# Performance work log

Measured on AMD Instinct MI355X. Metric: run time of the kernel, lower is better.

## Reference

```python
import jax, jax.numpy as jnp
import numpy as np
from jax import lax


def conv2d(x, w, b, pad):
    out = lax.conv_general_dilated(x, w, (1, 1), [(pad, pad), (pad, pad)],
                                   dimension_numbers=('NCHW', 'OIHW', 'NCHW'))
    return out + b[None, :, None, None]


def deform_conv3x3(src, offset, weight, bias):
    # torchvision.ops.deform_conv2d, 3x3 kernel, stride 1, pad 1, no mask.
    # src [B,C,H,W]; offset [B,18,H,W] laid out (y,x) per kernel pos, row-major.
    B, C, H, W = src.shape
    off = offset.reshape(B, 9, 2, H, W)
    ky, kx = jnp.meshgrid(jnp.arange(3) - 1, jnp.arange(3) - 1, indexing='ij')
    ky = ky.reshape(9).astype(src.dtype)
    kx = kx.reshape(9).astype(src.dtype)
    yy = jnp.arange(H, dtype=src.dtype)[:, None]
    xx = jnp.arange(W, dtype=src.dtype)[None, :]
    py = yy[None, None] + ky[None, :, None, None] + off[:, :, 0]  # [B,9,H,W]
    px = xx[None, None] + kx[None, :, None, None] + off[:, :, 1]
    y0 = jnp.floor(py)
    x0 = jnp.floor(px)
    wy1 = py - y0
    wx1 = px - x0

    def gather(yi, xi):
        valid = ((yi >= 0) & (yi < H) & (xi >= 0) & (xi < W)).astype(src.dtype)
        yc = jnp.clip(yi, 0, H - 1).astype(jnp.int32)
        xc = jnp.clip(xi, 0, W - 1).astype(jnp.int32)
        vals = jax.vmap(lambda s, a, c: s[:, a, c])(src, yc, xc)  # [B,C,9,H,W]
        return vals * valid[:, None]

    sampled = (gather(y0, x0) * ((1 - wy1) * (1 - wx1))[:, None]
               + gather(y0, x0 + 1) * ((1 - wy1) * wx1)[:, None]
               + gather(y0 + 1, x0) * (wy1 * (1 - wx1))[:, None]
               + gather(y0 + 1, x0 + 1) * (wy1 * wx1)[:, None])
    wk = weight.reshape(weight.shape[0], weight.shape[1], 9)
    return jnp.einsum('bckhw,ock->bohw', sampled, wk) + bias[None, :, None, None]


def setup_inputs() -> dict:
    key = jax.random.key(0)
    ks = jax.random.split(key, 16)
    B, C, H, W, N = 1, 256, 96, 96, 8
    current_feat = jax.random.normal(ks[0], (B, C, H, W), dtype=jnp.float32)
    neighbor_feats = jax.random.normal(ks[1], (N, B, C, H, W), dtype=jnp.float32)
    coord_diffs = jax.random.normal(ks[2], (N, 4), dtype=jnp.float32)
    align_w = jax.random.normal(ks[3], (C, C, 3, 3), dtype=jnp.float32) * 0.02
    align_b = jax.random.normal(ks[4], (C,), dtype=jnp.float32) * 0.02
    offset_w = jax.random.normal(ks[5], (18, 2 * C, 3, 3), dtype=jnp.float32) * 0.002
    offset_b = jax.random.normal(ks[6], (18,), dtype=jnp.float32) * 0.002
    gate1_w = jax.random.normal(ks[7], (C // 2, 2 * C, 3, 3), dtype=jnp.float32) * 0.02
    gate1_b = jax.random.normal(ks[8], (C // 2,), dtype=jnp.float32) * 0.02
    gate2_w = jax.random.normal(ks[9], (1, C // 2, 1, 1), dtype=jnp.float32) * 0.02
    gate2_b = jax.random.normal(ks[10], (1,), dtype=jnp.float32) * 0.02
    enc_w = jax.random.normal(ks[11], (C, 4), dtype=jnp.float32) * 0.1
    enc_b = jax.random.normal(ks[12], (C,), dtype=jnp.float32) * 0.1
    return dict(current_feat=current_feat, neighbor_feats=neighbor_feats,
                coord_diffs=coord_diffs, align_w=align_w, align_b=align_b,
                offset_w=offset_w, offset_b=offset_b, gate1_w=gate1_w,
                gate1_b=gate1_b, gate2_w=gate2_w, gate2_b=gate2_b,
                enc_w=enc_w, enc_b=enc_b)


def reference(current_feat, neighbor_feats, coord_diffs, align_w, align_b,
              offset_w, offset_b, gate1_w, gate1_b, gate2_w, gate2_b,
              enc_w, enc_b):
    B, C, H, W = current_feat.shape
    N = neighbor_feats.shape[0]
    aligned = []
    for n in range(N):  # fixed small neighbor set (<= 8)
        src = neighbor_feats[n]
        concat = jnp.concatenate([src, current_feat], axis=1)  # [B,2C,H,W]
        offset = conv2d(concat, offset_w, offset_b, 1)         # [B,18,H,W]
        aligned.append(deform_conv3x3(src, offset, align_w, align_b))
    all_feats = jnp.stack(aligned, axis=1)                     # [B,N,C,H,W]
    # coordinate embedding: Linear(4 -> C) per neighbor, shaped [1,N,C,1,1]
    coord_embs = (coord_diffs @ enc_w.T + enc_b)[None, :, :, None, None]
    cur_exp = jnp.broadcast_to(current_feat[:, None], (B, N, C, H, W))
    energy = jnp.concatenate([cur_exp, all_feats], axis=2).reshape(B * N, 2 * C, H, W)
    g = jax.nn.relu(conv2d(energy, gate1_w, gate1_b, 1))
    g = jax.nn.sigmoid(conv2d(g, gate2_w, gate2_b, 0))          # [B*N,1,H,W]
    weights = jax.nn.softmax(g.reshape(B, N, 1, H, W), axis=1)
    fused = (all_feats * weights + coord_embs).sum(axis=1)      # [B,C,H,W]
    return current_feat + 0.5 * fused
```

## Files before the change

kernel.cpp:

```cpp
#include <hip/hip_runtime.h>
#include <math.h>

#define CH   256
#define HH   96
#define WW   96
#define NN   8
#define HWSZ 9216
#define PLANE (HWSZ*CH)

typedef unsigned short u16;
typedef unsigned int   u32;
typedef short bf16x8 __attribute__((ext_vector_type(8)));
typedef float f32x4  __attribute__((ext_vector_type(4)));
typedef float f32x2  __attribute__((ext_vector_type(2)));

__device__ inline u16 f2bf(float f) {
    union { float f; u32 u; } v; v.f = f;
    u32 r = v.u + 0x7FFF + ((v.u >> 16) & 1);
    return (u16)(r >> 16);
}
__device__ inline float bflo(u32 u) {
    union { u32 u; float f; } v; v.u = u << 16; return v.f;
}
__device__ inline float bfhi(u32 u) {
    union { u32 u; float f; } v; v.u = u & 0xffff0000u; return v.f;
}
__device__ inline u32 pk2bf(float lo, float hi) {
    union { float f; u32 u; } a, b; a.f = lo; b.f = hi;
    u32 ra = a.u + 0x7FFF + ((a.u >> 16) & 1);
    u32 rb = b.u + 0x7FFF + ((b.u >> 16) & 1);
    return (ra >> 16) | (rb & 0xffff0000u);
}

__global__ void k_emb_sum(const float* __restrict__ cd,
                          const float* __restrict__ enc_w,
                          const float* __restrict__ enc_b,
                          float* __restrict__ emb)
{
    int c = threadIdx.x;
    float s = 0.f;
    for (int n = 0; n < NN; ++n) {
        float d = enc_b[c];
        #pragma unroll
        for (int j = 0; j < 4; ++j) d += cd[n*4 + j] * enc_w[c*4 + j];
        s += d;
    }
    emb[c] = s;
}

__global__ __launch_bounds__(256) void k_to_nhwc(const float* __restrict__ in,
                                                 u16* __restrict__ out)
{
    int n = blockIdx.y;
    int p0 = blockIdx.x * 64;
    int tid = threadIdx.x;
    __shared__ u16 T[64][262];

    int px4 = (tid & 15) * 4, cb = tid >> 4;
    for (int it = 0; it < 16; ++it) {
        int c = cb + it*16;
        float4 v = *reinterpret_cast<const float4*>(
            in + ((size_t)n*CH + c)*HWSZ + p0 + px4);
        T[px4+0][c] = f2bf(v.x);
        T[px4+1][c] = f2bf(v.y);
        T[px4+2][c] = f2bf(v.z);
        T[px4+3][c] = f2bf(v.w);
    }
    __syncthreads();
    int pxb = tid >> 5, ck = tid & 31;
    for (int it = 0; it < 8; ++it) {
        int p = pxb + it*8;
        *reinterpret_cast<int4*>(out + (size_t)n*PLANE + (size_t)(p0+p)*CH + ck*8) =
            *reinterpret_cast<const int4*>(&T[p][ck*8]);
    }
}

__global__ void k_pack_w(const float* __restrict__ w, u16* __restrict__ wp,
                         int O, int O_pad, int CIN, int order)
{
    int idx = blockIdx.x * 256 + threadIdx.x;
    int total = O_pad * CIN * 9;
    if (idx >= total) return;
    int o = idx / (CIN * 9);
    int K = idx % (CIN * 9);
    int tap = K / CIN, c = K % CIN;
    float v = (o < O) ? w[((size_t)o * CIN + c) * 9 + tap] : 0.f;
    int NKC = (CIN * 9) >> 5;
    int kc = order ? ((c >> 5)*9 + tap) : (tap*(CIN >> 5) + (c >> 5));
    int kl = c & 31;
    int lane = (kl >> 3) * 16 + (o & 15);
    size_t dstp = (((size_t)(o >> 4) * NKC + kc) * 64 + lane) * 8 + (kl & 7);
    wp[dstp] = f2bf(v);
}

template<int MTW, int EPI>
__global__ __launch_bounds__(512) void k_conv_nhwc(
    const u16* __restrict__ in0, long s0,
    const u16* __restrict__ in1, long s1,
    const u16* __restrict__ Wp, const float* __restrict__ b1,
    const float* __restrict__ g2w, const float* __restrict__ g2b,
    float* __restrict__ out)
{
    constexpr int NKC = 144, NCC = 16;
    int n = blockIdx.x, t = blockIdx.y;
    int tx0 = (t % 3) * 32, ty0 = (t / 3) * 8;
    int tid = threadIdx.x, lane = tid & 63, w = tid >> 6;
    int mh = w >> 2, pg = w & 3;
    int colq = lane >> 4;

    __shared__ __align__(16) u16 SB[340*40];
    __shared__ float gpart[8][64];

    f32x4 acc[MTW][4];
    #pragma unroll
    for (int mt = 0; mt < MTW; ++mt)
        #pragma unroll
        for (int nf = 0; nf < 4; ++nf)
            acc[mt][nf] = (f32x4){0.f,0.f,0.f,0.f};

    int bidx[4];
    #pragma unroll
    for (int nf = 0; nf < 4; ++nf) {
        int px = pg*64 + nf*16 + (lane & 15);
        int row = px >> 5, col = px & 31;
        bidx[nf] = ((row+1)*34 + (col+1))*40 + colq*8;
    }

    for (int cc = 0; cc < NCC; ++cc) {
        const u16* base = (cc < 8) ? in0 + (size_t)n*s0 + cc*32
                                   : in1 + (size_t)n*s1 + (cc-8)*32;
        for (int i = tid; i < 1360; i += 512) {
            int ph = i >> 2, q = i & 3;
            int r = ph / 34, col = ph - r*34;
            int y = ty0 - 1 + r, x = tx0 - 1 + col;
            bool v = ((unsigned)y < (unsigned)HH) && ((unsigned)x < (unsigned)WW);
            int off = v ? (y*WW + x)*CH : 0;
            int4 val = *reinterpret_cast<const int4*>(base + off + q*8);
            if (!v) val = make_int4(0,0,0,0);
            *reinterpret_cast<int4*>(&SB[ph*40 + q*8]) = val;
        }
        __syncthreads();
        #pragma unroll
        for (int tap = 0; tap < 9; ++tap) {
            int kc = tap*NCC + cc;
            bf16x8 a[MTW];
            #pragma unroll
            for (int mt = 0; mt < MTW; ++mt)
                a[mt] = *reinterpret_cast<const bf16x8*>(
                    Wp + (((size_t)(mh*MTW+mt)*NKC + kc)*64 + lane)*8);
            const int dy = tap/3 - 1, dx = tap%3 - 1;
            #pragma unroll
            for (int nf = 0; nf < 4; ++nf) {
                bf16x8 b = *reinterpret_cast<const bf16x8*>(
                    &SB[bidx[nf] + (dy*34 + dx)*40]);
                #pragma unroll
                for (int mt = 0; mt < MTW; ++mt)
                    acc[mt][nf] = __builtin_amdgcn_mfma_f32_16x16x32_bf16(
                                      a[mt], b, acc[mt][nf], 0, 0, 0);
            }
        }
        __syncthreads();
    }

    if (EPI == 0) {
        #pragma unroll
        for (int nf = 0; nf < 4; ++nf) {
            int px = pg*64 + nf*16 + (lane & 15);
            int gp = (ty0 + (px>>5))*WW + tx0 + (px & 31);
            #pragma unroll
            for (int mt = 0; mt < MTW; ++mt) {
                int o_base = (mh*MTW+mt)*16 + colq*4;
                #pragma unroll
                for (int r = 0; r < 4; ++r) {
                    int o = o_base + r;
                    if (o < 18)
                        out[((size_t)n*18 + o)*HWSZ + gp] = acc[mt][nf][r] + b1[o];
                }
            }
        }
    } else {
        float part[4];
        #pragma unroll
        for (int nf = 0; nf < 4; ++nf) {
            float s = 0.f;
            #pragma unroll
            for (int mt = 0; mt < MTW; ++mt) {
                int o_base = (mh*MTW+mt)*16 + colq*4;
                #pragma unroll
                for (int r = 0; r < 4; ++r) {
                    int o = o_base + r;
                    float vv = fmaxf(acc[mt][nf][r] + b1[o], 0.f);
                    s += vv * g2w[o];
                }
            }
            part[nf] = s;
        }
        #pragma unroll
        for (int nf = 0; nf < 4; ++nf) {
            part[nf] += __shfl_xor(part[nf], 16, 64);
            part[nf] += __shfl_xor(part[nf], 32, 64);
        }
        if (lane < 16) {
            #pragma unroll
            for (int nf = 0; nf < 4; ++nf)
                gpart[w][nf*16 + lane] = part[nf];
        }
        __syncthreads();
        if (tid < 256) {
            int pxl = tid & 63, pgg = tid >> 6;
            float s = gpart[pgg][pxl] + gpart[4 + pgg][pxl] + g2b[0];
            float g = 1.f / (1.f + expf(-s));
            int px = pgg*64 + pxl;
            int gp = (ty0 + (px>>5))*WW + tx0 + (px & 31);
            out[(size_t)n*HWSZ + gp] = g;
        }
    }
}

__global__ __launch_bounds__(256) void k_deform_nhwc(
    const u16* __restrict__ nbrh, const float* __restrict__ offs,
    const u16* __restrict__ Wp, const float* __restrict__ ab,
    u16* __restrict__ alig)
{
    constexpr int NKC = 72;
    int n = blockIdx.x, t = blockIdx.y;
    int tx0 = (t % 3) * 32, ty0 = (t / 3) * 2;
    int tid = threadIdx.x, lane = tid & 63, w = tid >> 6;
    int colq = lane >> 4;

    __shared__ __align__(16) char pool[29696];
    u16*    SB0  = (u16*)pool;
    u16*    SB1  = SB0 + 2816;
    int4*   cofs = (int4*)(pool + 11264);
    float4* cwt  = (float4*)(pool + 20480);

    const u16* src = nbrh + (size_t)n * PLANE;

    for (int i = tid; i < 576; i += 256) {
        int tt = i >> 6, p = i & 63;
        int y = ty0 + (p>>5), x = tx0 + (p & 31);
        int pp = y*WW + x;
        float oy = offs[((size_t)n*18 + 2*tt    )*HWSZ + pp];
        float ox = offs[((size_t)n*18 + 2*tt + 1)*HWSZ + pp];
        float py  = (float)y + (float)(tt/3 - 1) + oy;
        float pxx = (float)x + (float)(tt%3 - 1) + ox;
        py  = fminf(fmaxf(py,  -4.f), 100.f);
        pxx = fminf(fmaxf(pxx, -4.f), 100.f);
        float y0f = floorf(py), x0f = floorf(pxx);
        int y0 = (int)y0f, x0 = (int)x0f;
        float wy = py - y0f, wx = pxx - x0f;
        bool b00 = (y0 >= 0)  & (y0 < HH)   & (x0 >= 0)  & (x0 < WW);
        bool b01 = (y0 >= 0)  & (y0 < HH)   & (x0 >= -1) & (x0 < WW-1);
        bool b10 = (y0 >= -1) & (y0 < HH-1) & (x0 >= 0)  & (x0 < WW);
        bool b11 = (y0 >= -1) & (y0 < HH-1) & (x0 >= -1) & (x0 < WW-1);
        int a00 = (y0*WW + x0)*CH;
        int4 o4;
        o4.x = b00 ? a00             : 0;
        o4.y = b01 ? a00 + CH        : 0;
        o4.z = b10 ? a00 + WW*CH     : 0;
        o4.w = b11 ? a00 + WW*CH+CH  : 0;
        float4 w4;
        w4.x = b00 ? (1.f-wy)*(1.f-wx) : 0.f;
        w4.y = b01 ? (1.f-wy)*wx       : 0.f;
        w4.z = b10 ? wy*(1.f-wx)       : 0.f;
        w4.w = b11 ? wy*wx             : 0.f;
        cofs[i] = o4; cwt[i] = w4;
    }
    __syncthreads();

    f32x4 acc[4][4];
    #pragma unroll
    for (int mt = 0; mt < 4; ++mt)
        #pragma unroll
        for (int nf = 0; nf < 4; ++nf)
            acc[mt][nf] = (f32x4){0.f,0.f,0.f,0.f};

    int px = tid >> 2, chq = tid & 3;
    int sbw = px*44 + chq*8;
    int bb[4];
    #pragma unroll
    for (int nf = 0; nf < 4; ++nf)
        bb[nf] = (nf*16 + (lane & 15))*44 + colq*8;
    int c0base = chq*8;

    int4 o4; float4 w4;
    int4 crn[4];
    bf16x8 apf[4];

    auto loadCoord = [&](int kc) {
        int r = (kc >> 3)*64 + px;
        o4 = cofs[r]; w4 = cwt[r];
    };
    auto loadC = [&](int kc) {
        int c0 = (kc & 7)*32 + c0base;
        crn[0] = *reinterpret_cast<const int4*>(src + o4.x + c0);
        crn[1] = *reinterpret_cast<const int4*>(src + o4.y + c0);
        crn[2] = *reinterpret_cast<const int4*>(src + o4.z + c0);
        crn[3] = *reinterpret_cast<const int4*>(src + o4.w + c0);
    };
    auto loadA = [&](int kc) {
        #pragma unroll
        for (int mt = 0; mt < 4; ++mt)
            apf[mt] = *reinterpret_cast<const bf16x8*>(
                Wp + (((size_t)(w*4+mt)*NKC + kc)*64 + lane)*8);
    };
    auto bilerp = [&](float4 wt, const int4* q) -> int4 {
        f32x2 W00 = {wt.x, wt.x}, W01 = {wt.y, wt.y};
        f32x2 W10 = {wt.z, wt.z}, W11 = {wt.w, wt.w};
        int4 res;
        #pragma unroll
        for (int j = 0; j < 4; ++j) {
            u32 u00 = ((const u32*)&q[0])[j], u01 = ((const u32*)&q[1])[j];
            u32 u10 = ((const u32*)&q[2])[j], u11 = ((const u32*)&q[3])[j];
            f32x2 c00 = {bflo(u00), bfhi(u00)};
            f32x2 c01 = {bflo(u01), bfhi(u01)};
            f32x2 c10 = {bflo(u10), bfhi(u10)};
            f32x2 c11 = {bflo(u11), bfhi(u11)};
            f32x2 v = c00*W00;
            v += c01*W01;
            v += c10*W10;
            v += c11*W11;
            ((u32*)&res)[j] = pk2bf(v.x, v.y);
        }
        return res;
    };

    loadCoord(0);
    loadC(0);
    loadA(0);
    int cur = 0;
    for (int kc = 0; kc < NKC; ++kc) {
        int4 vpk = bilerp(w4, crn);
        u16* SBc = cur ? SB1 : SB0;
        *reinterpret_cast<int4*>(&SBc[sbw]) = vpk;
        bf16x8 a4[4];
        #pragma unroll
        for (int mt = 0; mt < 4; ++mt) a4[mt] = apf[mt];
        int kn = kc + 1;
        if (kn < NKC) {
            if ((kn & 7) == 0) loadCoord(kn);
            loadC(kn);
            loadA(kn);
        }
        __syncthreads();
        #pragma unroll
        for (int nf = 0; nf < 4; ++nf) {
            bf16x8 b = *reinterpret_cast<const bf16x8*>(&SBc[bb[nf]]);
            #pragma unroll
            for (int mt = 0; mt < 4; ++mt)
                acc[mt][nf] = __builtin_amdgcn_mfma_f32_16x16x32_bf16(
                                  a4[mt], b, acc[mt][nf], 0, 0, 0);
        }
        cur ^= 1;
    }

    __syncthreads();
    u16* TO = (u16*)pool;
    u16* aligp = alig + (size_t)n * PLANE;
    #pragma unroll
    for (int h = 0; h < 2; ++h) {
        #pragma unroll
        for (int sub = 0; sub < 2; ++sub) {
            int nf = 2*h + sub;
            int pl = sub*16 + (lane & 15);
            #pragma unroll
            for (int mt = 0; mt < 4; ++mt) {
                int o = (w*4+mt)*16 + colq*4;
                ushort4 v;
                v.x = f2bf(acc[mt][nf][0] + ab[o]);
                v.y = f2bf(acc[mt][nf][1] + ab[o+1]);
                v.z = f2bf(acc[mt][nf][2] + ab[o+2]);
                v.w = f2bf(acc[mt][nf][3] + ab[o+3]);
                *reinterpret_cast<ushort4*>(&TO[pl*264 + o]) = v;
            }
        }
        __syncthreads();
        #pragma unroll
        for (int it = 0; it < 4; ++it) {
            int i = tid + it*256;
            int pr = i >> 5, ck = i & 31;
            int nf = 2*h + (pr >> 4);
            int pxx = nf*16 + (pr & 15);
            int gp = (ty0 + (pxx>>5))*WW + tx0 + (pxx & 31);
            *reinterpret_cast<int4*>(aligp + (size_t)gp*CH + ck*8) =
                *reinterpret_cast<const int4*>(&TO[pr*264 + ck*8]);
        }
        __syncthreads();
    }
}

__global__ __launch_bounds__(256) void k_fuse_nhwc(
    const float* __restrict__ cur, const u16* __restrict__ alig,
    const float* __restrict__ g, const float* __restrict__ emb,
    float* __restrict__ out)
{
    int p0 = blockIdx.x * 32;
    int tid = threadIdx.x;
    __shared__ float wE[NN][32];
    __shared__ float trans[256][33];

    if (tid < 32) {
        int p = p0 + tid;
        float e[NN], m = -1e30f;
        #pragma unroll
        for (int n = 0; n < NN; ++n) { e[n] = g[n*HWSZ + p]; m = fmaxf(m, e[n]); }
        float se = 0.f;
        #pragma unroll
        for (int n = 0; n < NN; ++n) { e[n] = expf(e[n] - m); se += e[n]; }
        float inv = 1.f / se;
        #pragma unroll
        for (int n = 0; n < NN; ++n) wE[n][tid] = e[n] * inv;
    }
    __syncthreads();

    #pragma unroll
    for (int it = 0; it < 4; ++it) {
        int i = tid + it*256;
        int px = i >> 5, ck = i & 31;
        float a8[8];
        #pragma unroll
        for (int j = 0; j < 8; ++j) a8[j] = 0.f;
        #pragma unroll
        for (int n = 0; n < NN; ++n) {
            int4 v = *reinterpret_cast<const int4*>(
                &alig[((size_t)n*HWSZ + p0 + px)*CH + ck*8]);
            float f = wE[n][px];
            #pragma unroll
            for (int j4 = 0; j4 < 4; ++j4) {
                u32 u = ((const u32*)&v)[j4];
                a8[2*j4]   += bflo(u) * f;
                a8[2*j4+1] += bfhi(u) * f;
            }
        }
        #pragma unroll
        for (int j = 0; j < 8; ++j) {
            int c = ck*8 + j;
            trans[c][px ^ (c & 31)] = a8[j] + emb[c];
        }
    }
    __syncthreads();
    for (int it = 0; it < 32; ++it) {
        int c = (tid >> 5) + it*8, px = tid & 31;
        int idx = c*HWSZ + p0 + px;
        out[idx] = cur[idx] + 0.5f * trans[c][px ^ (c & 31)];
    }
}

extern "C" void kernel_launch(void* const* d_in, const int* in_sizes, int n_in,
                              void* d_out, int out_size, void* d_ws, size_t ws_size,
                              hipStream_t stream)
{
    const float* cur = (const float*)d_in[0];
    const float* nbr = (const float*)d_in[1];
    const float* cd  = (const float*)d_in[2];
    const float* aw  = (const float*)d_in[3];
    const float* ab  = (const float*)d_in[4];
    const float* ow  = (const float*)d_in[5];
    const float* ob  = (const float*)d_in[6];
    const float* g1w = (const float*)d_in[7];
    const float* g1b = (const float*)d_in[8];
    const float* g2w = (const float*)d_in[9];
    const float* g2b = (const float*)d_in[10];
    const float* ew  = (const float*)d_in[11];
    const float* eb  = (const float*)d_in[12];
    float* out = (float*)d_out;
    float* ws  = (float*)d_ws;

    float* offs = ws;
    float* gbuf = offs + 1327104;
    float* emb  = gbuf + 73728;
    u16* nbrh = (u16*)(emb + 256);
    u16* curh = nbrh + (size_t)NN*PLANE;
    u16* alig = curh + PLANE;
    u16* wpO  = alig + (size_t)NN*PLANE;
    u16* wpG  = wpO + 147456;
    u16* wpA  = wpG + 589824;

    k_emb_sum<<<dim3(1), dim3(256), 0, stream>>>(cd, ew, eb, emb);
    k_to_nhwc<<<dim3(144, 8), dim3(256), 0, stream>>>(nbr, nbrh);
    k_to_nhwc<<<dim3(144, 1), dim3(256), 0, stream>>>(cur, curh);
    k_pack_w<<<dim3((32*4608 + 255)/256), dim3(256), 0, stream>>>(ow, wpO, 18, 32, 512, 0);
    k_pack_w<<<dim3((128*4608 + 255)/256), dim3(256), 0, stream>>>(g1w, wpG, 128, 128, 512, 0);
    k_pack_w<<<dim3((256*2304 + 255)/256), dim3(256), 0, stream>>>(aw, wpA, 256, 256, 256, 0);

    k_conv_nhwc<1, 0><<<dim3(8, 36), dim3(512), 0, stream>>>(
        nbrh, (long)PLANE, curh, 0L, wpO, ob, nullptr, nullptr, offs);
    k_deform_nhwc<<<dim3(8, 144), dim3(256), 0, stream>>>(nbrh, offs, wpA, ab, alig);
    k_conv_nhwc<4, 1><<<dim3(8, 36), dim3(512), 0, stream>>>(
        curh, 0L, alig, (long)PLANE, wpG, g1b, g2w, g2b, gbuf);
    k_fuse_nhwc<<<dim3(288), dim3(256), 0, stream>>>(cur, alig, gbuf, emb, out);
}
```

Before: 447.5 us.

## Stage neighbor window in LDS for deformable conv when offsets stay local

The deformable conv kernel now checks per block whether every sampling point falls within a small window around the tile (3-pixel halo). If so, it loads that window for each 32-channel chunk into shared memory and does the bilinear gathers from LDS. Each thread then builds its own MFMA B fragment directly, with no per-step barrier round-trip through a staging buffer. Otherwise it falls back to global gathers with two barriers per step. The weight packing order changes (mode flag 1) so the K loop runs channel-chunk-major over the taps. The gain depends on offsets being small, as with the test inputs' conv-generated offsets, and the fallback path is slower than before.

```diff
diff --git a/kernel.cpp b/kernel.cpp
--- a/kernel.cpp
+++ b/kernel.cpp
@@ -226,16 +226,21 @@
     int n = blockIdx.x, t = blockIdx.y;
     int tx0 = (t % 3) * 32, ty0 = (t / 3) * 2;
     int tid = threadIdx.x, lane = tid & 63, w = tid >> 6;
-    int colq = lane >> 4;
-
-    __shared__ __align__(16) char pool[29696];
-    u16*    SB0  = (u16*)pool;
-    u16*    SB1  = SB0 + 2816;
-    int4*   cofs = (int4*)(pool + 11264);
-    float4* cwt  = (float4*)(pool + 20480);
+    int colq = lane >> 4, l15 = lane & 15;
+
+    __shared__ __align__(16) u16 LW[14080];
+    __shared__ __align__(16) float4 wtab[576];
+    __shared__ int bitab[576];
+    __shared__ int allok;
 
     const u16* src = nbrh + (size_t)n * PLANE;
-
+    int4* cofsS = (int4*)LW;
+    u16*  SBs   = LW + 4608;
+
+    if (tid == 0) allok = 1;
+    __syncthreads();
+
+    int myok = 1;
     for (int i = tid; i < 576; i += 256) {
         int tt = i >> 6, p = i & 63;
         int y = ty0 + (p>>5), x = tx0 + (p & 31);
@@ -253,20 +258,28 @@
         bool b01 = (y0 >= 0)  & (y0 < HH)   & (x0 >= -1) & (x0 < WW-1);
         bool b10 = (y0 >= -1) & (y0 < HH-1) & (x0 >= 0)  & (x0 < WW);
         bool b11 = (y0 >= -1) & (y0 < HH-1) & (x0 >= -1) & (x0 < WW-1);
+        float4 w4;
+        w4.x = b00 ? (1.f-wy)*(1.f-wx) : 0.f;
+        w4.y = b01 ? (1.f-wy)*wx       : 0.f;
+        w4.z = b10 ? wy*(1.f-wx)       : 0.f;
+        w4.w = b11 ? wy*wx             : 0.f;
+        wtab[i] = w4;
+        bool inw = (y0 >= ty0-3) & (y0 <= ty0+3) & (x0 >= tx0-3) & (x0 <= tx0+35);
+        int rr  = min(max(y0-(ty0-3), 0), 6);
+        int ccl = min(max(x0-(tx0-3), 0), 38);
+        bitab[i] = (rr*40 + ccl)*44;
+        if (!inw) myok = 0;
         int a00 = (y0*WW + x0)*CH;
         int4 o4;
         o4.x = b00 ? a00             : 0;
         o4.y = b01 ? a00 + CH        : 0;
         o4.z = b10 ? a00 + WW*CH     : 0;
         o4.w = b11 ? a00 + WW*CH+CH  : 0;
-        float4 w4;
-        w4.x = b00 ? (1.f-wy)*(1.f-wx) : 0.f;
-        w4.y = b01 ? (1.f-wy)*wx       : 0.f;
-        w4.z = b10 ? wy*(1.f-wx)       : 0.f;
-        w4.w = b11 ? wy*wx             : 0.f;
-        cofs[i] = o4; cwt[i] = w4;
-    }
+        cofsS[i] = o4;
+    }
+    if (!myok) atomicAnd(&allok, 0);
     __syncthreads();
+    bool fast = (allok != 0);
 
     f32x4 acc[4][4];
     #pragma unroll
@@ -275,43 +288,21 @@
         for (int nf = 0; nf < 4; ++nf)
             acc[mt][nf] = (f32x4){0.f,0.f,0.f,0.f};
 
-    int px = tid >> 2, chq = tid & 3;
-    int sbw = px*44 + chq*8;
-    int bb[4];
-    #pragma unroll
-    for (int nf = 0; nf < 4; ++nf)
-        bb[nf] = (nf*16 + (lane & 15))*44 + colq*8;
-    int c0base = chq*8;
-
-    int4 o4; float4 w4;
-    int4 crn[4];
     bf16x8 apf[4];
-
-    auto loadCoord = [&](int kc) {
-        int r = (kc >> 3)*64 + px;
-        o4 = cofs[r]; w4 = cwt[r];
-    };
-    auto loadC = [&](int kc) {
-        int c0 = (kc & 7)*32 + c0base;
-        crn[0] = *reinterpret_cast<const int4*>(src + o4.x + c0);
-        crn[1] = *reinterpret_cast<const int4*>(src + o4.y + c0);
-        crn[2] = *reinterpret_cast<const int4*>(src + o4.z + c0);
-        crn[3] = *reinterpret_cast<const int4*>(src + o4.w + c0);
-    };
     auto loadA = [&](int kc) {
         #pragma unroll
         for (int mt = 0; mt < 4; ++mt)
             apf[mt] = *reinterpret_cast<const bf16x8*>(
                 Wp + (((size_t)(w*4+mt)*NKC + kc)*64 + lane)*8);
     };
-    auto bilerp = [&](float4 wt, const int4* q) -> int4 {
+    auto bilerp = [&](float4 wt, int4 q0, int4 q1, int4 q2, int4 q3) -> bf16x8 {
         f32x2 W00 = {wt.x, wt.x}, W01 = {wt.y, wt.y};
         f32x2 W10 = {wt.z, wt.z}, W11 = {wt.w, wt.w};
         int4 res;
         #pragma unroll
         for (int j = 0; j < 4; ++j) {
-            u32 u00 = ((const u32*)&q[0])[j], u01 = ((const u32*)&q[1])[j];
-            u32 u10 = ((const u32*)&q[2])[j], u11 = ((const u32*)&q[3])[j];
+            u32 u00 = ((const u32*)&q0)[j], u01 = ((const u32*)&q1)[j];
+            u32 u10 = ((const u32*)&q2)[j], u11 = ((const u32*)&q3)[j];
             f32x2 c00 = {bflo(u00), bfhi(u00)};
             f32x2 c01 = {bflo(u01), bfhi(u01)};
             f32x2 c10 = {bflo(u10), bfhi(u10)};
@@ -322,47 +313,93 @@
             v += c11*W11;
             ((u32*)&res)[j] = pk2bf(v.x, v.y);
         }
-        return res;
+        union { int4 i4; bf16x8 b8; } cv; cv.i4 = res; return cv.b8;
     };
 
-    loadCoord(0);
-    loadC(0);
-    loadA(0);
-    int cur = 0;
-    for (int kc = 0; kc < NKC; ++kc) {
-        int4 vpk = bilerp(w4, crn);
-        u16* SBc = cur ? SB1 : SB0;
-        *reinterpret_cast<int4*>(&SBc[sbw]) = vpk;
-        bf16x8 a4[4];
-        #pragma unroll
-        for (int mt = 0; mt < 4; ++mt) a4[mt] = apf[mt];
-        int kn = kc + 1;
-        if (kn < NKC) {
-            if ((kn & 7) == 0) loadCoord(kn);
-            loadC(kn);
-            loadA(kn);
-        }
-        __syncthreads();
-        #pragma unroll
-        for (int nf = 0; nf < 4; ++nf) {
-            bf16x8 b = *reinterpret_cast<const bf16x8*>(&SBc[bb[nf]]);
-            #pragma unroll
-            for (int mt = 0; mt < 4; ++mt)
-                acc[mt][nf] = __builtin_amdgcn_mfma_f32_16x16x32_bf16(
-                                  a4[mt], b, acc[mt][nf], 0, 0, 0);
-        }
-        cur ^= 1;
+    if (fast) {
+        loadA(0);
+        for (int cc2 = 0; cc2 < 8; ++cc2) {
+            __syncthreads();
+            for (int u = tid; u < 1280; u += 256) {
+                int wp2 = u >> 2, q = u & 3;
+                int row = wp2 / 40, col = wp2 - row*40;
+                int y = ty0 - 3 + row, x = tx0 - 3 + col;
+                bool v = ((unsigned)y < (unsigned)HH) && ((unsigned)x < (unsigned)WW);
+                int4 val = v ? *reinterpret_cast<const int4*>(
+                                   src + (y*WW + x)*CH + cc2*32 + q*8)
+                             : make_int4(0,0,0,0);
+                *reinterpret_cast<int4*>(&LW[(row*40+col)*44 + q*8]) = val;
+            }
+            __syncthreads();
+            #pragma unroll
+            for (int tap = 0; tap < 9; ++tap) {
+                int kc = cc2*9 + tap;
+                bf16x8 a4[4];
+                #pragma unroll
+                for (int mt = 0; mt < 4; ++mt) a4[mt] = apf[mt];
+                if (kc + 1 < NKC) loadA(kc + 1);
+                #pragma unroll
+                for (int nf = 0; nf < 4; ++nf) {
+                    int r = tap*64 + nf*16 + l15;
+                    int base = bitab[r] + colq*8;
+                    float4 wt = wtab[r];
+                    int4 q0 = *reinterpret_cast<const int4*>(&LW[base]);
+                    int4 q1 = *reinterpret_cast<const int4*>(&LW[base + 44]);
+                    int4 q2 = *reinterpret_cast<const int4*>(&LW[base + 1760]);
+                    int4 q3 = *reinterpret_cast<const int4*>(&LW[base + 1804]);
+                    bf16x8 b = bilerp(wt, q0, q1, q2, q3);
+                    #pragma unroll
+                    for (int mt = 0; mt < 4; ++mt)
+                        acc[mt][nf] = __builtin_amdgcn_mfma_f32_16x16x32_bf16(
+                                          a4[mt], b, acc[mt][nf], 0, 0, 0);
+                }
+            }
+        }
+    } else {
+        int px = tid >> 2, chq = tid & 3;
+        int sbw = px*44 + chq*8;
+        int bb[4];
+        #pragma unroll
+        for (int nf = 0; nf < 4; ++nf)
+            bb[nf] = (nf*16 + l15)*44 + colq*8;
+        for (int cc2 = 0; cc2 < 8; ++cc2) {
+            for (int tap = 0; tap < 9; ++tap) {
+                int kc = cc2*9 + tap;
+                loadA(kc);
+                int r = tap*64 + px;
+                int4 o4 = cofsS[r];
+                float4 wt = wtab[r];
+                int c0 = cc2*32 + chq*8;
+                int4 q0 = *reinterpret_cast<const int4*>(src + o4.x + c0);
+                int4 q1 = *reinterpret_cast<const int4*>(src + o4.y + c0);
+                int4 q2 = *reinterpret_cast<const int4*>(src + o4.z + c0);
+                int4 q3 = *reinterpret_cast<const int4*>(src + o4.w + c0);
+                bf16x8 bv = bilerp(wt, q0, q1, q2, q3);
+                union { bf16x8 b8; int4 i4; } cv; cv.b8 = bv;
+                __syncthreads();
+                *reinterpret_cast<int4*>(&SBs[sbw]) = cv.i4;
+                __syncthreads();
+                #pragma unroll
+                for (int nf = 0; nf < 4; ++nf) {
+                    bf16x8 b = *reinterpret_cast<const bf16x8*>(&SBs[bb[nf]]);
+                    #pragma unroll
+                    for (int mt = 0; mt < 4; ++mt)
+                        acc[mt][nf] = __builtin_amdgcn_mfma_f32_16x16x32_bf16(
+                                          apf[mt], b, acc[mt][nf], 0, 0, 0);
+                }
+            }
+        }
     }
 
     __syncthreads();
-    u16* TO = (u16*)pool;
+    u16* TO = LW;
     u16* aligp = alig + (size_t)n * PLANE;
     #pragma unroll
     for (int h = 0; h < 2; ++h) {
         #pragma unroll
         for (int sub = 0; sub < 2; ++sub) {
             int nf = 2*h + sub;
-            int pl = sub*16 + (lane & 15);
+            int pl = sub*16 + l15;
             #pragma unroll
             for (int mt = 0; mt < 4; ++mt) {
                 int o = (w*4+mt)*16 + colq*4;
@@ -481,7 +518,7 @@
     k_to_nhwc<<<dim3(144, 1), dim3(256), 0, stream>>>(cur, curh);
     k_pack_w<<<dim3((32*4608 + 255)/256), dim3(256), 0, stream>>>(ow, wpO, 18, 32, 512, 0);
     k_pack_w<<<dim3((128*4608 + 255)/256), dim3(256), 0, stream>>>(g1w, wpG, 128, 128, 512, 0);
-    k_pack_w<<<dim3((256*2304 + 255)/256), dim3(256), 0, stream>>>(aw, wpA, 256, 256, 256, 0);
+    k_pack_w<<<dim3((256*2304 + 255)/256), dim3(256), 0, stream>>>(aw, wpA, 256, 256, 256, 1);
 
     k_conv_nhwc<1, 0><<<dim3(8, 36), dim3(512), 0, stream>>>(
         nbrh, (long)PLANE, curh, 0L, wpO, ob, nullptr, nullptr, offs);
```

Measured after the change: 901.6 us. 2.01x slower.
